# Optimization experiments

Measured on AMD Instinct MI355X. Metric: run time of the kernel, lower is better.

The kernel has to match this reference:

```python
import jax, jax.numpy as jnp
import numpy as np

V, E, H, L, B, S = 32000, 512, 1024, 2, 128, 256

def setup_inputs() -> dict:
    key = jax.random.key(0)
    ks = jax.random.split(key, 24)
    s = 0.02
    inp = {
        'input_token': jax.random.randint(ks[0], (B, 1), 0, V),
        'hidden': jax.random.normal(ks[1], (L, B, H), jnp.float32),
        'cell': jax.random.normal(ks[2], (L, B, H), jnp.float32),
        'encoder_outputs': jax.random.normal(ks[3], (B, S, H), jnp.float32),
        'embedding': jax.random.normal(ks[4], (V, E), jnp.float32) * s,
        'W1_w': jax.random.normal(ks[5], (H, H), jnp.float32) * s,
        'W1_b': jnp.zeros((H,), jnp.float32),
        'W2_w': jax.random.normal(ks[6], (H, H), jnp.float32) * s,
        'W2_b': jnp.zeros((H,), jnp.float32),
        'V_w': jax.random.normal(ks[7], (1, H), jnp.float32) * s,
        'V_b': jnp.zeros((1,), jnp.float32),
        'w_ih0': jax.random.normal(ks[8], (4 * H, E + H), jnp.float32) * s,
        'w_hh0': jax.random.normal(ks[9], (4 * H, H), jnp.float32) * s,
        'b_ih0': jnp.zeros((4 * H,), jnp.float32),
        'b_hh0': jnp.zeros((4 * H,), jnp.float32),
        'w_ih1': jax.random.normal(ks[10], (4 * H, H), jnp.float32) * s,
        'w_hh1': jax.random.normal(ks[11], (4 * H, H), jnp.float32) * s,
        'b_ih1': jnp.zeros((4 * H,), jnp.float32),
        'b_hh1': jnp.zeros((4 * H,), jnp.float32),
        'fc_w': jax.random.normal(ks[12], (V, 2 * H), jnp.float32) * s,
        'fc_b': jnp.zeros((V,), jnp.float32),
    }
    return inp


def _lstm_cell(x, h, c, w_ih, w_hh, b_ih, b_hh):
    # PyTorch gate order: i, f, g, o
    gates = x @ w_ih.T + b_ih + h @ w_hh.T + b_hh  # [B, 4H]
    i, f, g, o = jnp.split(gates, 4, axis=-1)
    i, f, o = jax.nn.sigmoid(i), jax.nn.sigmoid(f), jax.nn.sigmoid(o)
    g = jnp.tanh(g)
    c_new = f * c + i * g
    h_new = o * jnp.tanh(c_new)
    return h_new, c_new


def reference(input_token, hidden, cell, encoder_outputs, embedding,
              W1_w, W1_b, W2_w, W2_b, V_w, V_b,
              w_ih0, w_hh0, b_ih0, b_hh0, w_ih1, w_hh1, b_ih1, b_hh1,
              fc_w, fc_b):
    emb = embedding[input_token[:, 0]]                       # [B, E]
    h_top = hidden[-1]                                        # [B, H]
    # Bahdanau attention
    energy = jnp.tanh(encoder_outputs @ W1_w.T + W1_b
                      + (h_top @ W2_w.T + W2_b)[:, None, :])  # [B, S, H]
    scores = energy @ V_w.T + V_b                             # [B, S, 1]
    attn = jax.nn.softmax(scores, axis=1)                     # [B, S, 1]
    context = jnp.sum(attn * encoder_outputs, axis=1)         # [B, H]
    # single-step 2-layer LSTM
    x = jnp.concatenate([emb, context], axis=-1)              # [B, E+H]
    h0, c0 = _lstm_cell(x, hidden[0], cell[0], w_ih0, w_hh0, b_ih0, b_hh0)
    h1, c1 = _lstm_cell(h0, hidden[1], cell[1], w_ih1, w_hh1, b_ih1, b_hh1)
    # output projection
    logits = jnp.concatenate([h1, context], axis=-1) @ fc_w.T + fc_b  # [B, V]
    prediction = jax.nn.log_softmax(logits, axis=-1)
    new_hidden = jnp.stack([h0, h1])
    new_cell = jnp.stack([c0, c1])
    return prediction, new_hidden, new_cell, attn
```

## Files before the change

kernel.cpp:

```cpp
#include <hip/hip_runtime.h>

#define H_DIM 1024
#define B_DIM 128
#define S_DIM 256
#define V_DIM 32000
#define E_DIM 512

typedef __bf16 bf16_t;
typedef bf16_t bf16x8 __attribute__((ext_vector_type(8)));
typedef bf16_t bf16x4 __attribute__((ext_vector_type(4)));
typedef float floatx4 __attribute__((ext_vector_type(4)));

#define BM 128
#define BN 128
#define BK 64
#define LDK (BK + 8)

__device__ inline float fast_tanh(float x) {
    x = fminf(fmaxf(x, -15.f), 15.f);
    float e = __expf(2.f * x);
    return (e - 1.f) / (e + 1.f);
}
__device__ inline float sigmoidf_(float x) { return 1.f / (1.f + __expf(-x)); }
__device__ inline bf16x4 cvt4(float4 v) {
    return (bf16x4){(bf16_t)v.x, (bf16_t)v.y, (bf16_t)v.z, (bf16_t)v.w};
}
__device__ __forceinline__ void gload16(const bf16_t* g, bf16_t* l) {
    __builtin_amdgcn_global_load_lds(
        (const __attribute__((address_space(1))) void*)g,
        (__attribute__((address_space(3))) void*)l, 16, 0, 0);
}

__global__ __launch_bounds__(256) void gemm_scores_bf16(
    const bf16_t* __restrict__ A, const bf16_t* __restrict__ B,
    const float* __restrict__ bias1, const float* __restrict__ proj,
    const float* __restrict__ Vw, float* __restrict__ scores)
{
    __shared__ bf16_t As[128 * 64];
    __shared__ bf16_t Bs[128 * 64];

    const int tid  = threadIdx.x;
    const int wid  = tid >> 6;
    const int lane = tid & 63;

    const int orig = blockIdx.y * gridDim.x + blockIdx.x;
    const int cpx  = (gridDim.x * gridDim.y) >> 3;
    const int wg   = (orig & 7) * cpx + (orig >> 3);
    const int m0 = (wg >> 3) * BM;
    const int n0 = (wg & 7) * BN;

    const int wave_m = (wid & 1) * 64;
    const int wave_n = (wid >> 1) * 64;
    const int laneM  = lane & 15;
    const int laneG  = lane >> 4;

    const int srow = lane >> 3;
    const int pc   = lane & 7;

    floatx4 acc[4][4];
#pragma unroll
    for (int i = 0; i < 4; i++)
#pragma unroll
        for (int j = 0; j < 4; j++) acc[i][j] = (floatx4)0.f;

    for (int k0 = 0; k0 < H_DIM; k0 += BK) {
#pragma unroll
        for (int i = 0; i < 4; i++) {
            int r  = wid * 32 + i * 8 + srow;
            int lc = pc ^ (r & 7);
            gload16(A + (size_t)(m0 + r) * H_DIM + k0 + lc * 8,
                    As + (wid * 32 + i * 8) * 64);
        }
#pragma unroll
        for (int i = 0; i < 4; i++) {
            int r  = wid * 32 + i * 8 + srow;
            int lc = pc ^ (r & 7);
            gload16(B + (size_t)(n0 + r) * H_DIM + k0 + lc * 8,
                    Bs + (wid * 32 + i * 8) * 64);
        }
        __syncthreads();

#pragma unroll
        for (int kk = 0; kk < 2; kk++) {
            bf16x8 af[4], bfb[4];
#pragma unroll
            for (int mt = 0; mt < 4; mt++) {
                int ra = wave_m + mt * 16 + laneM;
                int pa = (kk * 4 + laneG) ^ (ra & 7);
                af[mt] = *(const bf16x8*)(&As[ra * 64 + pa * 8]);
            }
#pragma unroll
            for (int nt = 0; nt < 4; nt++) {
                int rb = wave_n + nt * 16 + laneM;
                int pb = (kk * 4 + laneG) ^ (rb & 7);
                bfb[nt] = *(const bf16x8*)(&Bs[rb * 64 + pb * 8]);
            }
#pragma unroll
            for (int mt = 0; mt < 4; mt++)
#pragma unroll
                for (int nt = 0; nt < 4; nt++)
                    acc[mt][nt] = __builtin_amdgcn_mfma_f32_16x16x32_bf16(
                        af[mt], bfb[nt], acc[mt][nt], 0, 0, 0);
        }
        __syncthreads();
    }

#pragma unroll
    for (int mt = 0; mt < 4; mt++) {
#pragma unroll
        for (int r = 0; r < 4; r++) {
            int m = m0 + wave_m + mt * 16 + (lane >> 4) * 4 + r;
            int b = m >> 8;
            float v = 0.f;
#pragma unroll
            for (int nt = 0; nt < 4; nt++) {
                int n = n0 + wave_n + nt * 16 + laneM;
                float t = acc[mt][nt][r] + bias1[n] + proj[(size_t)b * H_DIM + n];
                v += fast_tanh(t) * Vw[n];
            }
#pragma unroll
            for (int off = 1; off < 16; off <<= 1) v += __shfl_xor(v, off, 64);
            if (laneM == 0) atomicAdd(&scores[m], v);
        }
    }
}

template <int MODE>
__global__ __launch_bounds__(256) void gemm2(
    const float* __restrict__ A, int lda,
    const float* __restrict__ B1, int ldb1,
    const float* __restrict__ B2, int ldb2, int splitB,
    int K, int kChunk,
    float* __restrict__ C, int ldc,
    float* __restrict__ Cpart, long long partStride,
    const float* __restrict__ bias1, const float* __restrict__ bias2,
    const float* __restrict__ proj, const float* __restrict__ Vw,
    float* __restrict__ scores)
{
    __shared__ bf16_t As[BM][LDK];
    __shared__ bf16_t Bs[BN][LDK];

    const int tid  = threadIdx.x;
    const int wid  = tid >> 6;
    const int lane = tid & 63;

    int bx = blockIdx.x, by = blockIdx.y;
    if (MODE == 1) {
        int nwg  = gridDim.x * gridDim.y;
        int orig = by * gridDim.x + bx;
        int cpx  = nwg >> 3;
        int wg   = (orig & 7) * cpx + (orig >> 3);
        bx = wg % gridDim.x;
        by = wg / gridDim.x;
    }
    const int m0 = by * BM;
    const int n0 = bx * BN;

    const int wave_m = (wid & 1) * 64;
    const int wave_n = (wid >> 1) * 64;
    const int laneM  = lane & 15;
    const int laneK  = (lane >> 4) * 8;

    const int tk = (tid & 15) * 4;
    const int tr = tid >> 4;

    const int kStart = blockIdx.z * kChunk;
    const int kEnd   = min(K, kStart + kChunk);

    floatx4 acc[4][4];
#pragma unroll
    for (int i = 0; i < 4; i++)
#pragma unroll
        for (int j = 0; j < 4; j++) acc[i][j] = (floatx4)0.f;

    const float* Arow = A + (size_t)(m0 + tr) * lda + tk;

    float4 ar[8], br[8];
    auto loadA = [&](int k0) {
#pragma unroll
        for (int p = 0; p < 8; p++)
            ar[p] = *(const float4*)(Arow + (size_t)(p * 16) * lda + k0);
    };
    auto loadB = [&](int k0) {
        const float* Bp; size_t ldb; int kb;
        if (k0 < splitB) { Bp = B1; ldb = (size_t)ldb1; kb = k0 + tk; }
        else             { Bp = B2; ldb = (size_t)ldb2; kb = k0 - splitB + tk; }
        const float* Brow = Bp + (size_t)(n0 + tr) * ldb + kb;
#pragma unroll
        for (int p = 0; p < 8; p++)
            br[p] = *(const float4*)(Brow + (size_t)(p * 16) * ldb);
    };

    loadA(kStart); loadB(kStart);

    for (int k0 = kStart; k0 < kEnd; k0 += BK) {
#pragma unroll
        for (int p = 0; p < 8; p++) *(bf16x4*)(&As[tr + p * 16][tk]) = cvt4(ar[p]);
#pragma unroll
        for (int p = 0; p < 8; p++) *(bf16x4*)(&Bs[tr + p * 16][tk]) = cvt4(br[p]);
        __syncthreads();
        if (k0 + BK < kEnd) { loadA(k0 + BK); loadB(k0 + BK); }
#pragma unroll
        for (int kk = 0; kk < 2; kk++) {
            bf16x8 af[4], bfb[4];
#pragma unroll
            for (int mt = 0; mt < 4; mt++)
                af[mt] = *(const bf16x8*)(&As[wave_m + mt * 16 + laneM][kk * 32 + laneK]);
#pragma unroll
            for (int nt = 0; nt < 4; nt++)
                bfb[nt] = *(const bf16x8*)(&Bs[wave_n + nt * 16 + laneM][kk * 32 + laneK]);
#pragma unroll
            for (int mt = 0; mt < 4; mt++)
#pragma unroll
                for (int nt = 0; nt < 4; nt++)
                    acc[mt][nt] = __builtin_amdgcn_mfma_f32_16x16x32_bf16(
                        af[mt], bfb[nt], acc[mt][nt], 0, 0, 0);
        }
        __syncthreads();
    }

    if (MODE == 2 || MODE == 3) {
        const bool addb = (blockIdx.z == 0);
        float* dst = C;
        if (MODE == 3 && blockIdx.z > 0)
            dst = Cpart + (size_t)(blockIdx.z - 1) * partStride;
#pragma unroll
        for (int mt = 0; mt < 4; mt++) {
            int mrow = m0 + wave_m + mt * 16 + (lane >> 4) * 4;
#pragma unroll
            for (int nt = 0; nt < 4; nt++) {
                int n = n0 + wave_n + nt * 16 + laneM;
                float bsum = 0.f;
                if (addb) bsum = (bias1 ? bias1[n] : 0.f) + (bias2 ? bias2[n] : 0.f);
#pragma unroll
                for (int r = 0; r < 4; r++) {
                    float val = acc[mt][nt][r] + bsum;
                    if (MODE == 2) atomicAdd(&C[(size_t)(mrow + r) * ldc + n], val);
                    else           dst[(size_t)(mrow + r) * ldc + n] = val;
                }
            }
        }
    } else {
#pragma unroll
        for (int mt = 0; mt < 4; mt++) {
#pragma unroll
            for (int r = 0; r < 4; r++) {
                int m = m0 + wave_m + mt * 16 + (lane >> 4) * 4 + r;
                int b = m >> 8;
                float v = 0.f;
#pragma unroll
                for (int nt = 0; nt < 4; nt++) {
                    int n = n0 + wave_n + nt * 16 + laneM;
                    float t = acc[mt][nt][r] + bias1[n] + proj[(size_t)b * H_DIM + n];
                    v += fast_tanh(t) * Vw[n];
                }
#pragma unroll
                for (int off = 1; off < 16; off <<= 1) v += __shfl_xor(v, off, 64);
                if (laneM == 0) atomicAdd(&scores[m], v);
            }
        }
    }
}

__global__ void convert_kernel(const float* __restrict__ src,
                               bf16_t* __restrict__ dst, int n4) {
    int i = blockIdx.x * blockDim.x + threadIdx.x;
    int stride = gridDim.x * blockDim.x;
    for (; i < n4; i += stride) {
        float4 v = ((const float4*)src)[i];
        ((bf16x4*)dst)[i] = cvt4(v);
    }
}

template <typename T>
__global__ __launch_bounds__(256) void softmax_context_kernel(
    const T* __restrict__ enc, const float* __restrict__ scores,
    float* __restrict__ out_attn, float* __restrict__ x0, float* __restrict__ x2)
{
    __shared__ float red[256];
    __shared__ float a_s[256];
    int b = blockIdx.x, t = threadIdx.x;
    int half = blockIdx.y;
    float v = scores[b * S_DIM + t];
    red[t] = v; __syncthreads();
    for (int off = 128; off > 0; off >>= 1) {
        if (t < off) red[t] = fmaxf(red[t], red[t + off]);
        __syncthreads();
    }
    float mx = red[0]; __syncthreads();
    float e = __expf(v - mx);
    red[t] = e; __syncthreads();
    for (int off = 128; off > 0; off >>= 1) {
        if (t < off) red[t] += red[t + off];
        __syncthreads();
    }
    float a = e / red[0];
    if (half == 0) out_attn[b * S_DIM + t] = a;
    a_s[t] = a;
    __syncthreads();

    const int col = half * 512 + 2 * t;
    const T* base = enc + (size_t)b * S_DIM * H_DIM + col;
    float c0 = 0.f, c1 = 0.f;
#pragma unroll 4
    for (int s = 0; s < S_DIM; s++) {
        float aw = a_s[s];
        const T* row = base + (size_t)s * H_DIM;
        c0 += aw * (float)row[0];
        c1 += aw * (float)row[1];
    }
    x0[(size_t)b * 2560 + 512 + col]      = c0;
    x0[(size_t)b * 2560 + 512 + col + 1]  = c1;
    x2[(size_t)b * 2048 + 1024 + col]     = c0;
    x2[(size_t)b * 2048 + 1024 + col + 1] = c1;
}

__global__ void pack_misc_kernel(const int* __restrict__ tok,
                                 const float* __restrict__ emb_table,
                                 const float* __restrict__ hidden,
                                 float* __restrict__ x0, float* __restrict__ x1) {
    int b = blockIdx.y;
    int k = blockIdx.x * 256 + threadIdx.x;
    if (k < E_DIM)
        x0[(size_t)b * 2560 + k] = emb_table[(size_t)tok[b] * E_DIM + k];
    else if (k < E_DIM + H_DIM)
        x0[(size_t)b * 2560 + 1024 + k] = hidden[b * H_DIM + (k - E_DIM)];
    else
        x1[(size_t)b * 2048 + 1024 + (k - E_DIM - H_DIM)] =
            hidden[(size_t)B_DIM * H_DIM + b * H_DIM + (k - E_DIM - H_DIM)];
}

__global__ void lstm_cell_kernel(const float* __restrict__ gates,
                                 const float* __restrict__ gpart, int nExtra,
                                 long long partStride,
                                 const float* __restrict__ c_in,
                                 float* __restrict__ hx, int hx_stride,
                                 float* __restrict__ h_out,
                                 float* __restrict__ c_out) {
    int b = blockIdx.y;
    int n = blockIdx.x * 256 + threadIdx.x;
    size_t base = (size_t)b * 4 * H_DIM;
    float gi = gates[base + n];
    float gf = gates[base + H_DIM + n];
    float gg = gates[base + 2 * H_DIM + n];
    float go = gates[base + 3 * H_DIM + n];
    for (int p = 0; p < nExtra; p++) {
        size_t pb = (size_t)p * partStride + base;
        gi += gpart[pb + n];
        gf += gpart[pb + H_DIM + n];
        gg += gpart[pb + 2 * H_DIM + n];
        go += gpart[pb + 3 * H_DIM + n];
    }
    float i = sigmoidf_(gi), f = sigmoidf_(gf), o = sigmoidf_(go);
    float g = fast_tanh(gg);
    float c = f * c_in[b * H_DIM + n] + i * g;
    float h = o * fast_tanh(c);
    hx[(size_t)b * hx_stride + n] = h;
    h_out[b * H_DIM + n] = h;
    c_out[b * H_DIM + n] = c;
}

__global__ __launch_bounds__(1024) void log_softmax_kernel(
    float* __restrict__ pred, const float* __restrict__ part) {
    __shared__ float red[1024];
    int b = blockIdx.x, t = threadIdx.x;
    float lv[32];
    float mx = -1e30f;
#pragma unroll
    for (int j = 0; j < 32; j++) {
        int v = t + j * 1024;
        float x = -1e30f;
        if (v < V_DIM) {
            x = pred[(size_t)b * V_DIM + v];
            if (part) x += part[(size_t)b * V_DIM + v];
        }
        lv[j] = x;
        mx = fmaxf(mx, x);
    }
    red[t] = mx; __syncthreads();
    for (int off = 512; off > 0; off >>= 1) {
        if (t < off) red[t] = fmaxf(red[t], red[t + off]);
        __syncthreads();
    }
    mx = red[0]; __syncthreads();
    float s = 0.f;
#pragma unroll
    for (int j = 0; j < 32; j++) s += __expf(lv[j] - mx);
    red[t] = s; __syncthreads();
    for (int off = 512; off > 0; off >>= 1) {
        if (t < off) red[t] += red[t + off];
        __syncthreads();
    }
    float lse = mx + __logf(red[0]);
#pragma unroll
    for (int j = 0; j < 32; j++) {
        int v = t + j * 1024;
        if (v < V_DIM) pred[(size_t)b * V_DIM + v] = lv[j] - lse;
    }
}

extern "C" void kernel_launch(void* const* d_in, const int* in_sizes, int n_in,
                              void* d_out, int out_size, void* d_ws, size_t ws_size,
                              hipStream_t stream) {
    const int*   tok    = (const int*)  d_in[0];
    const float* hidden = (const float*)d_in[1];
    const float* cell   = (const float*)d_in[2];
    const float* enc    = (const float*)d_in[3];
    const float* embt   = (const float*)d_in[4];
    const float* W1w    = (const float*)d_in[5];
    const float* W1b    = (const float*)d_in[6];
    const float* W2w    = (const float*)d_in[7];
    const float* W2b    = (const float*)d_in[8];
    const float* Vw     = (const float*)d_in[9];
    const float* wih0 = (const float*)d_in[11];
    const float* whh0 = (const float*)d_in[12];
    const float* bih0 = (const float*)d_in[13];
    const float* bhh0 = (const float*)d_in[14];
    const float* wih1 = (const float*)d_in[15];
    const float* whh1 = (const float*)d_in[16];
    const float* bih1 = (const float*)d_in[17];
    const float* bhh1 = (const float*)d_in[18];
    const float* fcw  = (const float*)d_in[19];
    const float* fcb  = (const float*)d_in[20];

    float* out        = (float*)d_out;
    float* pred       = out;
    float* out_hidden = out + (size_t)B_DIM * V_DIM;
    float* out_cell   = out_hidden + 2 * B_DIM * H_DIM;
    float* out_attn   = out_cell + 2 * B_DIM * H_DIM;

    float* ws      = (float*)d_ws;
    float* scores  = ws;
    float* proj    = ws + 32768;
    float* gatesA  = ws + 163840;
    float* gatesB  = ws + 688128;
    float* x0      = ws + 1212416;
    float* x1      = ws + 1540096;
    float* x2      = ws + 1802240;
    float* gAp     = ws + 2064384;
    float* gBp     = ws + 3637248;
    float* fcpart  = ws + 5210112;
    bf16_t* encbf  = (bf16_t*)(ws + 9306112);
    bf16_t* W1bf   = (bf16_t*)(ws + 26083328);

    const bool pathA = ws_size >= (size_t)26607616 * 4;
    const bool pathB = !pathA && ws_size >= (size_t)9306112 * 4 + 16384000;
    const bool split = pathA || pathB;

    dim3 blk(256);

    if (split)
        hipMemsetAsync(ws, 0, (size_t)163840 * 4, stream);
    else
        hipMemsetAsync(ws, 0, (size_t)1212416 * 4, stream);

    pack_misc_kernel<<<dim3(10, B_DIM), blk, 0, stream>>>(tok, embt, hidden, x0, x1);

    gemm2<2><<<dim3(8, 1, 2), blk, 0, stream>>>(
        hidden + (size_t)B_DIM * H_DIM, H_DIM, W2w, H_DIM, nullptr, 0, H_DIM,
        H_DIM, 512, proj, H_DIM, nullptr, 0, W2b, nullptr, nullptr, nullptr, nullptr);

    if (pathA) {
        convert_kernel<<<4096, blk, 0, stream>>>(enc, encbf, 8388608);
        convert_kernel<<<1024, blk, 0, stream>>>(W1w, W1bf, 262144);
        gemm_scores_bf16<<<dim3(8, 256), blk, 0, stream>>>(
            encbf, W1bf, W1b, proj, Vw, scores);
        softmax_context_kernel<bf16_t><<<dim3(B_DIM, 2), 256, 0, stream>>>(
            encbf, scores, out_attn, x0, x2);
    } else {
        gemm2<1><<<dim3(8, 256, 1), blk, 0, stream>>>(
            enc, H_DIM, W1w, H_DIM, nullptr, 0, H_DIM,
            H_DIM, H_DIM, nullptr, 0, nullptr, 0, W1b, nullptr, proj, Vw, scores);
        softmax_context_kernel<float><<<dim3(B_DIM, 2), 256, 0, stream>>>(
            enc, scores, out_attn, x0, x2);
    }

    if (split) {
        gemm2<3><<<dim3(32, 1, 4), blk, 0, stream>>>(
            x0, 2560, wih0, 1536, whh0, H_DIM, 1536, 2560, 640,
            gatesA, 4096, gAp, 524288, bih0, bhh0, nullptr, nullptr, nullptr);
        lstm_cell_kernel<<<dim3(4, B_DIM), blk, 0, stream>>>(
            gatesA, gAp, 3, 524288, cell, x1, 2048, out_hidden, out_cell);
    } else {
        gemm2<2><<<dim3(32, 1, 4), blk, 0, stream>>>(
            x0, 2560, wih0, 1536, whh0, H_DIM, 1536, 2560, 640,
            gatesA, 4096, nullptr, 0, bih0, bhh0, nullptr, nullptr, nullptr);
        lstm_cell_kernel<<<dim3(4, B_DIM), blk, 0, stream>>>(
            gatesA, nullptr, 0, 0, cell, x1, 2048, out_hidden, out_cell);
    }

    if (split) {
        gemm2<3><<<dim3(32, 1, 4), blk, 0, stream>>>(
            x1, 2048, wih1, H_DIM, whh1, H_DIM, H_DIM, 2048, 512,
            gatesB, 4096, gBp, 524288, bih1, bhh1, nullptr, nullptr, nullptr);
        lstm_cell_kernel<<<dim3(4, B_DIM), blk, 0, stream>>>(
            gatesB, gBp, 3, 524288, cell + (size_t)B_DIM * H_DIM, x2, 2048,
            out_hidden + (size_t)B_DIM * H_DIM, out_cell + (size_t)B_DIM * H_DIM);
    } else {
        gemm2<2><<<dim3(32, 1, 4), blk, 0, stream>>>(
            x1, 2048, wih1, H_DIM, whh1, H_DIM, H_DIM, 2048, 512,
            gatesB, 4096, nullptr, 0, bih1, bhh1, nullptr, nullptr, nullptr);
        lstm_cell_kernel<<<dim3(4, B_DIM), blk, 0, stream>>>(
            gatesB, nullptr, 0, 0, cell + (size_t)B_DIM * H_DIM, x2, 2048,
            out_hidden + (size_t)B_DIM * H_DIM, out_cell + (size_t)B_DIM * H_DIM);
    }

    if (split) {
        gemm2<3><<<dim3(250, 1, 2), blk, 0, stream>>>(
            x2, 2048, fcw, 2048, nullptr, 0, 2048, 2048, 1024,
            pred, V_DIM, fcpart, 4096000, fcb, nullptr, nullptr, nullptr, nullptr);
        log_softmax_kernel<<<B_DIM, 1024, 0, stream>>>(pred, fcpart);
    } else {
        gemm2<3><<<dim3(250, 1, 1), blk, 0, stream>>>(
            x2, 2048, fcw, 2048, nullptr, 0, 2048, 2048, 2048,
            pred, V_DIM, nullptr, 0, fcb, nullptr, nullptr, nullptr, nullptr);
        log_softmax_kernel<<<B_DIM, 1024, 0, stream>>>(pred, nullptr);
    }
}
```

Measured before the change: 758.9 us.

## Fuse prep work into one kernel and deepen split-K for LSTM GEMMs

On the large-workspace path, a single prep kernel replaces the memset, pack, W2 projection GEMM and the two bf16 conversion kernels. It computes the W2 projection with per-wave dot products, zeroes the scores buffer, and grid-strides over the conversions and input packing. The LSTM gate GEMMs go from 4-way to 8-way split-K using the fcpart buffer for partials, to get more parallelism. The goal is fewer launches and better occupancy, at the cost of a scalar-style W2 GEMV that rereads W2 for each batch row and more partial-sum traffic.

Result: slower. 903.1 us (+19.0%).

```diff
diff --git a/kernel.cpp b/kernel.cpp
--- a/kernel.cpp
+++ b/kernel.cpp
@@ -29,6 +29,68 @@
     __builtin_amdgcn_global_load_lds(
         (const __attribute__((address_space(1))) void*)g,
         (__attribute__((address_space(3))) void*)l, 16, 0, 0);
+}
+
+__global__ __launch_bounds__(256) void prep_kernel(
+    const float* __restrict__ enc, bf16_t* __restrict__ encbf,
+    const float* __restrict__ W1w, bf16_t* __restrict__ W1bf,
+    const int* __restrict__ tok, const float* __restrict__ embt,
+    const float* __restrict__ hidden,
+    float* __restrict__ x0, float* __restrict__ x1,
+    const float* __restrict__ W2w, const float* __restrict__ W2b,
+    float* __restrict__ proj, float* __restrict__ scores)
+{
+    const int t = threadIdx.x;
+    if (blockIdx.x < 128) {
+        const int b = blockIdx.x;
+        scores[b * 256 + t] = 0.f;
+        const float* h = hidden + (size_t)B_DIM * H_DIM + (size_t)b * H_DIM;
+        const int wv = t >> 6, ln = t & 63;
+        float4 hr[4];
+#pragma unroll
+        for (int c = 0; c < 4; c++)
+            hr[c] = *(const float4*)(h + c * 256 + ln * 4);
+        for (int n = wv; n < H_DIM; n += 4) {
+            const float* wrow = W2w + (size_t)n * H_DIM;
+            float s = 0.f;
+#pragma unroll
+            for (int c = 0; c < 4; c++) {
+                float4 w4 = *(const float4*)(wrow + c * 256 + ln * 4);
+                s += w4.x * hr[c].x + w4.y * hr[c].y + w4.z * hr[c].z + w4.w * hr[c].w;
+            }
+#pragma unroll
+            for (int off = 1; off < 64; off <<= 1) s += __shfl_xor(s, off, 64);
+            if (ln == 0) proj[(size_t)b * H_DIM + n] = s + W2b[n];
+        }
+        return;
+    }
+    const long long N_ENC = 8388608, N_W1 = 262144, N_EMB = 16384, N_H0 = 32768, N_H1 = 32768;
+    const long long total = N_ENC + N_W1 + N_EMB + N_H0 + N_H1;
+    const long long stride = (long long)(gridDim.x - 128) * 256;
+    for (long long i = (long long)(blockIdx.x - 128) * 256 + t; i < total; i += stride) {
+        if (i < N_ENC) {
+            float4 v = ((const float4*)enc)[i];
+            ((bf16x4*)encbf)[i] = cvt4(v);
+        } else if (i < N_ENC + N_W1) {
+            long long k = i - N_ENC;
+            ((bf16x4*)W1bf)[k] = cvt4(((const float4*)W1w)[k]);
+        } else if (i < N_ENC + N_W1 + N_EMB) {
+            long long k = i - N_ENC - N_W1;
+            int b = (int)(k >> 7), j = (int)(k & 127);
+            ((float4*)(x0 + (size_t)b * 2560))[j] =
+                ((const float4*)(embt + (size_t)tok[b] * E_DIM))[j];
+        } else if (i < N_ENC + N_W1 + N_EMB + N_H0) {
+            long long k = i - N_ENC - N_W1 - N_EMB;
+            int b = (int)(k >> 8), j = (int)(k & 255);
+            ((float4*)(x0 + (size_t)b * 2560 + 1536))[j] =
+                ((const float4*)(hidden + (size_t)b * H_DIM))[j];
+        } else {
+            long long k = i - N_ENC - N_W1 - N_EMB - N_H0;
+            int b = (int)(k >> 8), j = (int)(k & 255);
+            ((float4*)(x1 + (size_t)b * 2048 + 1024))[j] =
+                ((const float4*)(hidden + (size_t)B_DIM * H_DIM + (size_t)b * H_DIM))[j];
+        }
+    }
 }
 
 __global__ __launch_bounds__(256) void gemm_scores_bf16(
@@ -449,6 +511,35 @@
 
     dim3 blk(256);
 
+    if (pathA) {
+        prep_kernel<<<dim3(2176), blk, 0, stream>>>(
+            enc, encbf, W1w, W1bf, tok, embt, hidden, x0, x1, W2w, W2b, proj, scores);
+
+        gemm_scores_bf16<<<dim3(8, 256), blk, 0, stream>>>(
+            encbf, W1bf, W1b, proj, Vw, scores);
+        softmax_context_kernel<bf16_t><<<dim3(B_DIM, 2), 256, 0, stream>>>(
+            encbf, scores, out_attn, x0, x2);
+
+        gemm2<3><<<dim3(32, 1, 8), blk, 0, stream>>>(
+            x0, 2560, wih0, 1536, whh0, H_DIM, 1536, 2560, 320,
+            gatesA, 4096, fcpart, 524288, bih0, bhh0, nullptr, nullptr, nullptr);
+        lstm_cell_kernel<<<dim3(4, B_DIM), blk, 0, stream>>>(
+            gatesA, fcpart, 7, 524288, cell, x1, 2048, out_hidden, out_cell);
+
+        gemm2<3><<<dim3(32, 1, 8), blk, 0, stream>>>(
+            x1, 2048, wih1, H_DIM, whh1, H_DIM, H_DIM, 2048, 256,
+            gatesB, 4096, fcpart, 524288, bih1, bhh1, nullptr, nullptr, nullptr);
+        lstm_cell_kernel<<<dim3(4, B_DIM), blk, 0, stream>>>(
+            gatesB, fcpart, 7, 524288, cell + (size_t)B_DIM * H_DIM, x2, 2048,
+            out_hidden + (size_t)B_DIM * H_DIM, out_cell + (size_t)B_DIM * H_DIM);
+
+        gemm2<3><<<dim3(250, 1, 2), blk, 0, stream>>>(
+            x2, 2048, fcw, 2048, nullptr, 0, 2048, 2048, 1024,
+            pred, V_DIM, fcpart, 4096000, fcb, nullptr, nullptr, nullptr, nullptr);
+        log_softmax_kernel<<<B_DIM, 1024, 0, stream>>>(pred, fcpart);
+        return;
+    }
+
     if (split)
         hipMemsetAsync(ws, 0, (size_t)163840 * 4, stream);
     else
@@ -460,20 +551,11 @@
         hidden + (size_t)B_DIM * H_DIM, H_DIM, W2w, H_DIM, nullptr, 0, H_DIM,
         H_DIM, 512, proj, H_DIM, nullptr, 0, W2b, nullptr, nullptr, nullptr, nullptr);
 
-    if (pathA) {
-        convert_kernel<<<4096, blk, 0, stream>>>(enc, encbf, 8388608);
-        convert_kernel<<<1024, blk, 0, stream>>>(W1w, W1bf, 262144);
-        gemm_scores_bf16<<<dim3(8, 256), blk, 0, stream>>>(
-            encbf, W1bf, W1b, proj, Vw, scores);
-        softmax_context_kernel<bf16_t><<<dim3(B_DIM, 2), 256, 0, stream>>>(
-            encbf, scores, out_attn, x0, x2);
-    } else {
-        gemm2<1><<<dim3(8, 256, 1), blk, 0, stream>>>(
-            enc, H_DIM, W1w, H_DIM, nullptr, 0, H_DIM,
-            H_DIM, H_DIM, nullptr, 0, nullptr, 0, W1b, nullptr, proj, Vw, scores);
-        softmax_context_kernel<float><<<dim3(B_DIM, 2), 256, 0, stream>>>(
-            enc, scores, out_attn, x0, x2);
-    }
+    gemm2<1><<<dim3(8, 256, 1), blk, 0, stream>>>(
+        enc, H_DIM, W1w, H_DIM, nullptr, 0, H_DIM,
+        H_DIM, H_DIM, nullptr, 0, nullptr, 0, W1b, nullptr, proj, Vw, scores);
+    softmax_context_kernel<float><<<dim3(B_DIM, 2), 256, 0, stream>>>(
+        enc, scores, out_attn, x0, x2);
 
     if (split) {
         gemm2<3><<<dim3(32, 1, 4), blk, 0, stream>>>(
```
